# Optimization experiments

Measured on AMD Instinct MI355X. Metric: run time of the kernel, lower is better.

Reference implementation:

```python
import jax, jax.numpy as jnp
import numpy as np

N_NODES = 100000


def gcn_conv(x, edge_index, W, b, n_nodes):
    """PyG GCNConv: add self-loops, symmetric deg^-1/2 normalization,
    linear transform, scatter-add aggregate, bias."""
    src, dst = edge_index[0], edge_index[1]
    # add self-loops
    loop = jnp.arange(n_nodes, dtype=edge_index.dtype)
    src = jnp.concatenate([src, loop])
    dst = jnp.concatenate([dst, loop])
    # transform first (in_dim >= out_dim ordering used by PyG)
    h = x @ W  # [N, out]
    # symmetric normalization from in-degree (incl. self-loops)
    ones = jnp.ones(src.shape[0], dtype=x.dtype)
    deg = jax.ops.segment_sum(ones, dst, num_segments=n_nodes)
    dinv = jnp.where(deg > 0, jax.lax.rsqrt(deg), 0.0).astype(x.dtype)
    norm = dinv[src] * dinv[dst]  # [E+N]
    msg = h[src] * norm[:, None]  # gather + scale
    out = jax.ops.segment_sum(msg, dst, num_segments=n_nodes)
    return out + b


def setup_inputs() -> dict:
    key = jax.random.key(0)
    k1, k2, k3, k4 = jax.random.split(key, 4)
    n, e = N_NODES, 1600000
    d_in, d_hid, n_cls = 256, 256, 64
    x = jax.random.normal(k1, (n, d_in), dtype=jnp.float32)
    edge_index = jax.random.randint(k2, (2, e), 0, n, dtype=jnp.int64)
    W1 = jax.random.normal(k3, (d_in, d_hid), dtype=jnp.float32) / np.sqrt(d_in)
    b1 = jnp.zeros((d_hid,), dtype=jnp.float32)
    W2 = jax.random.normal(k4, (d_hid, n_cls), dtype=jnp.float32) / np.sqrt(d_hid)
    b2 = jnp.zeros((n_cls,), dtype=jnp.float32)
    return {"x": x, "edge_index": edge_index, "W1": W1, "b1": b1, "W2": W2, "b2": b2}


def reference(x, edge_index, W1, b1, W2, b2):
    n = x.shape[0]
    h = jax.nn.relu(gcn_conv(x, edge_index, W1, b1, n))
    # dropout is identity in eval mode (training=False)
    logits = gcn_conv(h, edge_index, W2, b2, n)
    return jax.nn.log_softmax(logits, axis=1)
```

## Files before the change

kernel.cpp:

```cpp
#include <hip/hip_runtime.h>
#include <math.h>


typedef __attribute__((ext_vector_type(8))) short bf16x8;
typedef __attribute__((ext_vector_type(4))) float f32x4;

__device__ inline unsigned short f2bf(float f) {
    union { float f; unsigned int u; } v; v.f = f;
    unsigned int r = v.u + 0x7fffu + ((v.u >> 16) & 1u);
    return (unsigned short)(r >> 16);
}
__device__ inline float bf2f_lo(unsigned int u) {
    union { unsigned int u; float f; } v; v.u = u << 16; return v.f;
}
__device__ inline float bf2f_hi(unsigned int u) {
    union { unsigned int u; float f; } v; v.u = u & 0xffff0000u; return v.f;
}

__device__ inline void acc8(float* acc, uint4 q, float w) {
    acc[0] += bf2f_lo(q.x) * w; acc[1] += bf2f_hi(q.x) * w;
    acc[2] += bf2f_lo(q.y) * w; acc[3] += bf2f_hi(q.y) * w;
    acc[4] += bf2f_lo(q.z) * w; acc[5] += bf2f_hi(q.z) * w;
    acc[6] += bf2f_lo(q.w) * w; acc[7] += bf2f_hi(q.w) * w;
}

__global__ __launch_bounds__(256) void deg_rank_kernel(
    const int* __restrict__ dst, int E, int* __restrict__ cnt,
    int* __restrict__ rank) {
    int e = blockIdx.x * blockDim.x + threadIdx.x;
    if (e < E) rank[e] = atomicAdd(&cnt[dst[e]], 1);
}

__global__ __launch_bounds__(256) void scan_part1_kernel(
    const int* __restrict__ cnt, int* __restrict__ bsum, int N) {
    __shared__ int s[256];
    const int tid = threadIdx.x;
    int base = blockIdx.x * 1024 + tid * 4;
    int v = 0;
#pragma unroll
    for (int j = 0; j < 4; ++j)
        if (base + j < N) v += cnt[base + j];
    s[tid] = v;
    __syncthreads();
    for (int off = 128; off > 0; off >>= 1) {
        if (tid < off) s[tid] += s[tid + off];
        __syncthreads();
    }
    if (tid == 0) bsum[blockIdx.x] = s[0];
}

__global__ __launch_bounds__(1024) void scan_part2_kernel(
    const int* __restrict__ bsum, int* __restrict__ boffs, int NB,
    int* __restrict__ row_ptr, int N) {
    __shared__ int s[1024];
    const int tid = threadIdx.x;
    int v = (tid < NB) ? bsum[tid] : 0;
    s[tid] = v;
    __syncthreads();
    for (int off = 1; off < 1024; off <<= 1) {
        int t = (tid >= off) ? s[tid - off] : 0;
        __syncthreads();
        if (tid >= off) s[tid] += t;
        __syncthreads();
    }
    if (tid < NB) boffs[tid] = s[tid] - v;
    if (tid == 1023) row_ptr[N] = s[1023];
}

__global__ __launch_bounds__(256) void scan_part3_kernel(
    const int* __restrict__ cnt, const int* __restrict__ boffs,
    int* __restrict__ row_ptr, int N) {
    __shared__ int s[256];
    const int tid = threadIdx.x;
    int base = blockIdx.x * 1024 + tid * 4;
    int c[4];
    int v = 0;
#pragma unroll
    for (int j = 0; j < 4; ++j) {
        c[j] = (base + j < N) ? cnt[base + j] : 0;
        v += c[j];
    }
    s[tid] = v;
    __syncthreads();
    for (int off = 1; off < 256; off <<= 1) {
        int t = (tid >= off) ? s[tid - off] : 0;
        __syncthreads();
        if (tid >= off) s[tid] += t;
        __syncthreads();
    }
    int run = boffs[blockIdx.x] + s[tid] - v;
#pragma unroll
    for (int j = 0; j < 4; ++j) {
        if (base + j < N) {
            row_ptr[base + j] = run;
            run += c[j];
        }
    }
}

__global__ __launch_bounds__(256) void scatter_kernel(
    const int* __restrict__ src, const int* __restrict__ dst,
    const int* __restrict__ rank, const int* __restrict__ cnt,
    const int* __restrict__ row_ptr, int2* __restrict__ csr_ew, int E) {
    int e = blockIdx.x * blockDim.x + threadIdx.x;
    if (e >= E) return;
    int s = src[e], d = dst[e];
    float w = rsqrtf((float)cnt[s] + 1.0f) * rsqrtf((float)cnt[d] + 1.0f);
    int pos = row_ptr[d] + rank[e];
    int2 rec;
    rec.x = s;
    rec.y = __float_as_int(w);
    csr_ew[pos] = rec;
}

__global__ __launch_bounds__(256) void castw_kernel(
    const float* __restrict__ W1, const float* __restrict__ W2,
    unsigned short* __restrict__ W1t, unsigned short* __restrict__ W2t) {
    int i = blockIdx.x * 256 + threadIdx.x;
    if (i < 65536) {
        int n = i >> 8, k = i & 255;
        W1t[i] = f2bf(W1[(size_t)k * 256 + n]);
    } else if (i < 65536 + 16384) {
        int j = i - 65536;
        int n = j >> 8, k = j & 255;
        W2t[j] = f2bf(W2[(size_t)k * 64 + n]);
    }
}

__global__ __launch_bounds__(256) void gemm1_kernel(
    const float* __restrict__ A, const unsigned short* __restrict__ Bt,
    unsigned short* __restrict__ C, int M) {
    __shared__ unsigned short As[128][32];
    __shared__ unsigned short Bs[256][32];

    const int tid = threadIdx.x;
    const int wave = tid >> 6, lane = tid & 63;
    const int quad = lane >> 4, l15 = lane & 15;
    const int m0 = blockIdx.x * 128;

    f32x4 acc[8][4] = {};

    const int arow = tid >> 1;
    const int akk  = (tid & 1) << 4;
    const int gr = m0 + arow;

    for (int k0 = 0; k0 < 256; k0 += 32) {
        float4 a0 = make_float4(0.f,0.f,0.f,0.f), a1 = a0, a2 = a0, a3 = a0;
        if (gr < M) {
            const float* ap = &A[(size_t)gr * 256 + k0 + akk];
            a0 = *(const float4*)&ap[0];
            a1 = *(const float4*)&ap[4];
            a2 = *(const float4*)&ap[8];
            a3 = *(const float4*)&ap[12];
        }
        bf16x8 av0, av1;
        av0[0] = (short)f2bf(a0.x); av0[1] = (short)f2bf(a0.y);
        av0[2] = (short)f2bf(a0.z); av0[3] = (short)f2bf(a0.w);
        av0[4] = (short)f2bf(a1.x); av0[5] = (short)f2bf(a1.y);
        av0[6] = (short)f2bf(a1.z); av0[7] = (short)f2bf(a1.w);
        av1[0] = (short)f2bf(a2.x); av1[1] = (short)f2bf(a2.y);
        av1[2] = (short)f2bf(a2.z); av1[3] = (short)f2bf(a2.w);
        av1[4] = (short)f2bf(a3.x); av1[5] = (short)f2bf(a3.y);
        av1[6] = (short)f2bf(a3.z); av1[7] = (short)f2bf(a3.w);
        *(bf16x8*)&As[arow][akk]     = av0;
        *(bf16x8*)&As[arow][akk + 8] = av1;

        const unsigned short* bsrc = &Bt[(size_t)tid * 256 + k0];
        *(bf16x8*)&Bs[tid][0]  = *(const bf16x8*)&bsrc[0];
        *(bf16x8*)&Bs[tid][8]  = *(const bf16x8*)&bsrc[8];
        *(bf16x8*)&Bs[tid][16] = *(const bf16x8*)&bsrc[16];
        *(bf16x8*)&Bs[tid][24] = *(const bf16x8*)&bsrc[24];
        __syncthreads();

        bf16x8 bfv[4];
#pragma unroll
        for (int nt = 0; nt < 4; ++nt)
            bfv[nt] = *(const bf16x8*)&Bs[wave * 64 + nt * 16 + l15][quad * 8];
#pragma unroll
        for (int mt = 0; mt < 8; ++mt) {
            bf16x8 af = *(const bf16x8*)&As[mt * 16 + l15][quad * 8];
#pragma unroll
            for (int nt = 0; nt < 4; ++nt)
                acc[mt][nt] = __builtin_amdgcn_mfma_f32_16x16x32_bf16(
                    af, bfv[nt], acc[mt][nt], 0, 0, 0);
        }
        __syncthreads();
    }

#pragma unroll
    for (int mt = 0; mt < 8; ++mt) {
#pragma unroll
        for (int nt = 0; nt < 4; ++nt) {
            int gcol = wave * 64 + nt * 16 + l15;
#pragma unroll
            for (int r = 0; r < 4; ++r) {
                int grow = m0 + mt * 16 + quad * 4 + r;
                if (grow < M)
                    C[(size_t)grow * 256 + gcol] = f2bf(acc[mt][nt][r]);
            }
        }
    }
}

__global__ __launch_bounds__(256) void aggfused_kernel(
    const uint4* __restrict__ h,
    const int2* __restrict__ ew,
    const int* __restrict__ row_ptr, const int* __restrict__ cnt,
    const float* __restrict__ bias, const unsigned short* __restrict__ W2t,
    unsigned short* __restrict__ h2b, int N) {
    __shared__ unsigned short As[16][264];

    const int tid = threadIdx.x;
    const int wave = tid >> 6, lane = tid & 63;
    const int half = lane >> 5;
    const int c = lane & 31;
    const int node0 = blockIdx.x * 16;

    for (int i = 0; i < 4; ++i) {
        const int local = wave * 4 + i;
        const int node = node0 + local;
        float acc[8] = {0.f, 0.f, 0.f, 0.f, 0.f, 0.f, 0.f, 0.f};
        if (node < N) {
            float dv = rsqrtf((float)cnt[node] + 1.0f);
            float w0 = dv * dv;
            uint4 qs = h[(size_t)node * 32 + c];
            const int beg = row_ptr[node], end = row_ptr[node + 1];
            acc8(acc, qs, half == 0 ? w0 : 0.f);
            if (beg < end) {
                const int last = end - 1;
                int2 r0 = ew[min(beg + half,     last)];
                int2 r1 = ew[min(beg + 2 + half, last)];
                int2 r2 = ew[min(beg + 4 + half, last)];
                int2 r3 = ew[min(beg + 6 + half, last)];
                for (int e = beg; e < end; e += 8) {
                    float we0 = (e + half     < end) ? __int_as_float(r0.y) : 0.f;
                    float we1 = (e + 2 + half < end) ? __int_as_float(r1.y) : 0.f;
                    float we2 = (e + 4 + half < end) ? __int_as_float(r2.y) : 0.f;
                    float we3 = (e + 6 + half < end) ? __int_as_float(r3.y) : 0.f;
                    uint4 q0 = h[(size_t)r0.x * 32 + c];
                    uint4 q1 = h[(size_t)r1.x * 32 + c];
                    uint4 q2 = h[(size_t)r2.x * 32 + c];
                    uint4 q3 = h[(size_t)r3.x * 32 + c];
                    const int en = e + 8;
                    int2 n0 = ew[min(en + half,     last)];
                    int2 n1 = ew[min(en + 2 + half, last)];
                    int2 n2 = ew[min(en + 4 + half, last)];
                    int2 n3 = ew[min(en + 6 + half, last)];
                    acc8(acc, q0, we0);
                    acc8(acc, q1, we1);
                    acc8(acc, q2, we2);
                    acc8(acc, q3, we3);
                    r0 = n0; r1 = n1; r2 = n2; r3 = n3;
                }
            }
        }
#pragma unroll
        for (int k = 0; k < 8; ++k) acc[k] += __shfl_xor(acc[k], 32, 64);

        if (half == 0) {
            float4 b0 = *(const float4*)&bias[c * 8];
            float4 b1 = *(const float4*)&bias[c * 8 + 4];
            unsigned int o0 = f2bf(fmaxf(acc[0] + b0.x, 0.f));
            unsigned int o1 = f2bf(fmaxf(acc[1] + b0.y, 0.f));
            unsigned int o2 = f2bf(fmaxf(acc[2] + b0.z, 0.f));
            unsigned int o3 = f2bf(fmaxf(acc[3] + b0.w, 0.f));
            unsigned int o4 = f2bf(fmaxf(acc[4] + b1.x, 0.f));
            unsigned int o5 = f2bf(fmaxf(acc[5] + b1.y, 0.f));
            unsigned int o6 = f2bf(fmaxf(acc[6] + b1.z, 0.f));
            unsigned int o7 = f2bf(fmaxf(acc[7] + b1.w, 0.f));
            uint4 ov;
            ov.x = o0 | (o1 << 16);
            ov.y = o2 | (o3 << 16);
            ov.z = o4 | (o5 << 16);
            ov.w = o6 | (o7 << 16);
            *(uint4*)&As[local][c * 8] = ov;
        }
    }
    __syncthreads();

    const int quad = lane >> 4, l15 = lane & 15;
    f32x4 accd = {};
#pragma unroll
    for (int k0 = 0; k0 < 8; ++k0) {
        bf16x8 af = *(const bf16x8*)&As[l15][k0 * 32 + quad * 8];
        bf16x8 bf = *(const bf16x8*)&W2t[(size_t)(wave * 16 + l15) * 256 +
                                         k0 * 32 + quad * 8];
        accd = __builtin_amdgcn_mfma_f32_16x16x32_bf16(af, bf, accd, 0, 0, 0);
    }
#pragma unroll
    for (int r = 0; r < 4; ++r) {
        int node = node0 + quad * 4 + r;
        if (node < N)
            h2b[(size_t)node * 64 + wave * 16 + l15] = f2bf(accd[r]);
    }
}

__global__ __launch_bounds__(256) void agg64_kernel(
    const uint4* __restrict__ h,
    const int2* __restrict__ ew, const int* __restrict__ row_ptr,
    const int* __restrict__ cnt, const float* __restrict__ bias,
    float* __restrict__ out, int N) {
    const int node = blockIdx.x * 4 + (threadIdx.x >> 6);
    if (node >= N) return;
    const int lane = threadIdx.x & 63;
    const int g = lane >> 3;
    const int c = lane & 7;

    float dv = rsqrtf((float)cnt[node] + 1.0f);
    float w0 = dv * dv;

    float acc[8] = {0.f, 0.f, 0.f, 0.f, 0.f, 0.f, 0.f, 0.f};
    {
        uint4 q = h[(size_t)node * 8 + c];
        acc8(acc, q, g == 0 ? w0 : 0.f);
    }

    const int beg = row_ptr[node], end = row_ptr[node + 1];
    if (beg < end) {
        const int last = end - 1;
        int2 r0 = ew[min(beg + g,     last)];
        int2 r1 = ew[min(beg + 8 + g, last)];
        for (int e = beg; e < end; e += 16) {
            float wa = (e + g     < end) ? __int_as_float(r0.y) : 0.f;
            float wb = (e + 8 + g < end) ? __int_as_float(r1.y) : 0.f;
            uint4 q0 = h[(size_t)r0.x * 8 + c];
            uint4 q1 = h[(size_t)r1.x * 8 + c];
            const int en = e + 16;
            int2 n0 = ew[min(en + g,     last)];
            int2 n1 = ew[min(en + 8 + g, last)];
            acc8(acc, q0, wa);
            acc8(acc, q1, wb);
            r0 = n0; r1 = n1;
        }
    }

#pragma unroll
    for (int k = 0; k < 8; ++k) {
        acc[k] += __shfl_xor(acc[k], 8, 64);
        acc[k] += __shfl_xor(acc[k], 16, 64);
        acc[k] += __shfl_xor(acc[k], 32, 64);
    }

    float4 b0 = *(const float4*)&bias[c * 8];
    float4 b1 = *(const float4*)&bias[c * 8 + 4];
    float v[8];
    v[0] = acc[0] + b0.x; v[1] = acc[1] + b0.y;
    v[2] = acc[2] + b0.z; v[3] = acc[3] + b0.w;
    v[4] = acc[4] + b1.x; v[5] = acc[5] + b1.y;
    v[6] = acc[6] + b1.z; v[7] = acc[7] + b1.w;

    float m = v[0];
#pragma unroll
    for (int k = 1; k < 8; ++k) m = fmaxf(m, v[k]);
    m = fmaxf(m, __shfl_xor(m, 1, 64));
    m = fmaxf(m, __shfl_xor(m, 2, 64));
    m = fmaxf(m, __shfl_xor(m, 4, 64));
    float s = 0.f;
#pragma unroll
    for (int k = 0; k < 8; ++k) s += expf(v[k] - m);
    s += __shfl_xor(s, 1, 64);
    s += __shfl_xor(s, 2, 64);
    s += __shfl_xor(s, 4, 64);
    float ls = m + logf(s);

    if (g == 0) {
        float4 o0, o1;
        o0.x = v[0] - ls; o0.y = v[1] - ls; o0.z = v[2] - ls; o0.w = v[3] - ls;
        o1.x = v[4] - ls; o1.y = v[5] - ls; o1.z = v[6] - ls; o1.w = v[7] - ls;
        *(float4*)&out[(size_t)node * 64 + c * 8] = o0;
        *(float4*)&out[(size_t)node * 64 + c * 8 + 4] = o1;
    }
}

extern "C" void kernel_launch(void* const* d_in, const int* in_sizes, int n_in,
                              void* d_out, int out_size, void* d_ws, size_t ws_size,
                              hipStream_t stream) {
    const float* x  = (const float*)d_in[0];
    const int*   ei = (const int*)d_in[1];
    const float* W1 = (const float*)d_in[2];
    const float* b1 = (const float*)d_in[3];
    const float* W2 = (const float*)d_in[4];
    const float* b2 = (const float*)d_in[5];
    float* out = (float*)d_out;

    const int N = in_sizes[0] / 256;
    const int E = in_sizes[1] / 2;
    const int NP = 102400;
    const int NB = (N + 1023) / 1024;

    char* ws = (char*)d_ws;
    int*   cnt     = (int*)ws;                 ws += (size_t)NP * 4;
    int*   rank    = (int*)ws;                 ws += (size_t)E * 4;
    int*   row_ptr = (int*)ws;                 ws += (size_t)(NP + 4) * 4;
    int*   bsum    = (int*)ws;                 ws += (size_t)1024 * 4;
    int*   boffs   = (int*)ws;                 ws += (size_t)1024 * 4;
    int2*  csr_ew  = (int2*)ws;                ws += (size_t)E * 8;
    unsigned short* W1t   = (unsigned short*)ws; ws += (size_t)256 * 256 * 2;
    unsigned short* W2t   = (unsigned short*)ws; ws += (size_t)256 * 64 * 2;
    unsigned short* h1b   = (unsigned short*)ws; ws += (size_t)N * 256 * 2;
    unsigned short* h2b   = (unsigned short*)ws; ws += (size_t)N * 64 * 2;

    hipMemsetAsync(cnt, 0, (size_t)N * sizeof(int), stream);

    deg_rank_kernel<<<(E + 255) / 256, 256, 0, stream>>>(ei + E, E, cnt, rank);
    scan_part1_kernel<<<NB, 256, 0, stream>>>(cnt, bsum, N);
    scan_part2_kernel<<<1, 1024, 0, stream>>>(bsum, boffs, NB, row_ptr, N);
    scan_part3_kernel<<<NB, 256, 0, stream>>>(cnt, boffs, row_ptr, N);
    scatter_kernel<<<(E + 255) / 256, 256, 0, stream>>>(
        ei, ei + E, rank, cnt, row_ptr, csr_ew, E);

    castw_kernel<<<(65536 + 16384 + 255) / 256, 256, 0, stream>>>(W1, W2, W1t, W2t);

    gemm1_kernel<<<(N + 127) / 128, 256, 0, stream>>>(x, W1t, h1b, N);

    aggfused_kernel<<<(N + 15) / 16, 256, 0, stream>>>(
        (const uint4*)h1b, csr_ew, row_ptr, cnt, b1, W2t, h2b, N);

    agg64_kernel<<<(N + 3) / 4, 256, 0, stream>>>(
        (const uint4*)h2b, csr_ew, row_ptr, cnt, b2, out, N);
}
```

Before: 539.2 us.

## Fold symmetric normalization into GEMM epilogue and drop per-edge weights

Precomputes deg^-1/2 once per node during the scan, then pre-scales the transformed features by the source-node factor in the GEMM and layer-1 epilogues. The destination factor is applied once per node after aggregation. This removes the per-edge weight from the CSR, halving edge-record bandwidth to plain int source indices. Padding is handled with a zeroed dummy row N instead of clamped indices, and nontemporal loads and stores are added on streaming accesses. The trade-off is that bf16 rounding now happens on pre-scaled values, and the zero row must be written each call.

```diff
diff --git a/kernel.cpp b/kernel.cpp
--- a/kernel.cpp
+++ b/kernel.cpp
@@ -17,18 +17,22 @@
     union { unsigned int u; float f; } v; v.u = u & 0xffff0000u; return v.f;
 }
 
-__device__ inline void acc8(float* acc, uint4 q, float w) {
-    acc[0] += bf2f_lo(q.x) * w; acc[1] += bf2f_hi(q.x) * w;
-    acc[2] += bf2f_lo(q.y) * w; acc[3] += bf2f_hi(q.y) * w;
-    acc[4] += bf2f_lo(q.z) * w; acc[5] += bf2f_hi(q.z) * w;
-    acc[6] += bf2f_lo(q.w) * w; acc[7] += bf2f_hi(q.w) * w;
+__device__ inline void acc8a(float* acc, uint4 q) {
+    acc[0] += bf2f_lo(q.x); acc[1] += bf2f_hi(q.x);
+    acc[2] += bf2f_lo(q.y); acc[3] += bf2f_hi(q.y);
+    acc[4] += bf2f_lo(q.z); acc[5] += bf2f_hi(q.z);
+    acc[6] += bf2f_lo(q.w); acc[7] += bf2f_hi(q.w);
 }
 
 __global__ __launch_bounds__(256) void deg_rank_kernel(
     const int* __restrict__ dst, int E, int* __restrict__ cnt,
     int* __restrict__ rank) {
     int e = blockIdx.x * blockDim.x + threadIdx.x;
-    if (e < E) rank[e] = atomicAdd(&cnt[dst[e]], 1);
+    if (e < E) {
+        int d = __builtin_nontemporal_load(&dst[e]);
+        int r = atomicAdd(&cnt[d], 1);
+        __builtin_nontemporal_store(r, &rank[e]);
+    }
 }
 
 __global__ __launch_bounds__(256) void scan_part1_kernel(
@@ -69,7 +73,7 @@
 
 __global__ __launch_bounds__(256) void scan_part3_kernel(
     const int* __restrict__ cnt, const int* __restrict__ boffs,
-    int* __restrict__ row_ptr, int N) {
+    int* __restrict__ row_ptr, float* __restrict__ dv, int N) {
     __shared__ int s[256];
     const int tid = threadIdx.x;
     int base = blockIdx.x * 1024 + tid * 4;
@@ -93,6 +97,7 @@
     for (int j = 0; j < 4; ++j) {
         if (base + j < N) {
             row_ptr[base + j] = run;
+            dv[base + j] = rsqrtf((float)c[j] + 1.0f);
             run += c[j];
         }
     }
@@ -100,22 +105,21 @@
 
 __global__ __launch_bounds__(256) void scatter_kernel(
     const int* __restrict__ src, const int* __restrict__ dst,
-    const int* __restrict__ rank, const int* __restrict__ cnt,
-    const int* __restrict__ row_ptr, int2* __restrict__ csr_ew, int E) {
+    const int* __restrict__ rank, const int* __restrict__ row_ptr,
+    int* __restrict__ csr_src, int E) {
     int e = blockIdx.x * blockDim.x + threadIdx.x;
     if (e >= E) return;
-    int s = src[e], d = dst[e];
-    float w = rsqrtf((float)cnt[s] + 1.0f) * rsqrtf((float)cnt[d] + 1.0f);
-    int pos = row_ptr[d] + rank[e];
-    int2 rec;
-    rec.x = s;
-    rec.y = __float_as_int(w);
-    csr_ew[pos] = rec;
+    int d = __builtin_nontemporal_load(&dst[e]);
+    int s = __builtin_nontemporal_load(&src[e]);
+    int r = __builtin_nontemporal_load(&rank[e]);
+    csr_src[row_ptr[d] + r] = s;
 }
 
 __global__ __launch_bounds__(256) void castw_kernel(
     const float* __restrict__ W1, const float* __restrict__ W2,
-    unsigned short* __restrict__ W1t, unsigned short* __restrict__ W2t) {
+    unsigned short* __restrict__ W1t, unsigned short* __restrict__ W2t,
+    unsigned short* __restrict__ h1s, unsigned short* __restrict__ h2s,
+    int N) {
     int i = blockIdx.x * 256 + threadIdx.x;
     if (i < 65536) {
         int n = i >> 8, k = i & 255;
@@ -124,12 +128,16 @@
         int j = i - 65536;
         int n = j >> 8, k = j & 255;
         W2t[j] = f2bf(W2[(size_t)k * 64 + n]);
+    } else {
+        int t = i - (65536 + 16384);
+        h1s[(size_t)N * 256 + t] = 0;
+        if (t < 64) h2s[(size_t)N * 64 + t] = 0;
     }
 }
 
 __global__ __launch_bounds__(256) void gemm1_kernel(
     const float* __restrict__ A, const unsigned short* __restrict__ Bt,
-    unsigned short* __restrict__ C, int M) {
+    const float* __restrict__ dv, unsigned short* __restrict__ C, int M) {
     __shared__ unsigned short As[128][32];
     __shared__ unsigned short Bs[256][32];
 
@@ -145,23 +153,23 @@
     const int gr = m0 + arow;
 
     for (int k0 = 0; k0 < 256; k0 += 32) {
-        float4 a0 = make_float4(0.f,0.f,0.f,0.f), a1 = a0, a2 = a0, a3 = a0;
+        f32x4 a0 = {0.f, 0.f, 0.f, 0.f}, a1 = a0, a2 = a0, a3 = a0;
         if (gr < M) {
-            const float* ap = &A[(size_t)gr * 256 + k0 + akk];
-            a0 = *(const float4*)&ap[0];
-            a1 = *(const float4*)&ap[4];
-            a2 = *(const float4*)&ap[8];
-            a3 = *(const float4*)&ap[12];
+            const f32x4* ap = (const f32x4*)&A[(size_t)gr * 256 + k0 + akk];
+            a0 = __builtin_nontemporal_load(&ap[0]);
+            a1 = __builtin_nontemporal_load(&ap[1]);
+            a2 = __builtin_nontemporal_load(&ap[2]);
+            a3 = __builtin_nontemporal_load(&ap[3]);
         }
         bf16x8 av0, av1;
-        av0[0] = (short)f2bf(a0.x); av0[1] = (short)f2bf(a0.y);
-        av0[2] = (short)f2bf(a0.z); av0[3] = (short)f2bf(a0.w);
-        av0[4] = (short)f2bf(a1.x); av0[5] = (short)f2bf(a1.y);
-        av0[6] = (short)f2bf(a1.z); av0[7] = (short)f2bf(a1.w);
-        av1[0] = (short)f2bf(a2.x); av1[1] = (short)f2bf(a2.y);
-        av1[2] = (short)f2bf(a2.z); av1[3] = (short)f2bf(a2.w);
-        av1[4] = (short)f2bf(a3.x); av1[5] = (short)f2bf(a3.y);
-        av1[6] = (short)f2bf(a3.z); av1[7] = (short)f2bf(a3.w);
+        av0[0] = (short)f2bf(a0[0]); av0[1] = (short)f2bf(a0[1]);
+        av0[2] = (short)f2bf(a0[2]); av0[3] = (short)f2bf(a0[3]);
+        av0[4] = (short)f2bf(a1[0]); av0[5] = (short)f2bf(a1[1]);
+        av0[6] = (short)f2bf(a1[2]); av0[7] = (short)f2bf(a1[3]);
+        av1[0] = (short)f2bf(a2[0]); av1[1] = (short)f2bf(a2[1]);
+        av1[2] = (short)f2bf(a2[2]); av1[3] = (short)f2bf(a2[3]);
+        av1[4] = (short)f2bf(a3[0]); av1[5] = (short)f2bf(a3[1]);
+        av1[6] = (short)f2bf(a3[2]); av1[7] = (short)f2bf(a3[3]);
         *(bf16x8*)&As[arow][akk]     = av0;
         *(bf16x8*)&As[arow][akk + 8] = av1;
 
@@ -190,13 +198,14 @@
 #pragma unroll
     for (int mt = 0; mt < 8; ++mt) {
 #pragma unroll
-        for (int nt = 0; nt < 4; ++nt) {
-            int gcol = wave * 64 + nt * 16 + l15;
-#pragma unroll
-            for (int r = 0; r < 4; ++r) {
-                int grow = m0 + mt * 16 + quad * 4 + r;
-                if (grow < M)
-                    C[(size_t)grow * 256 + gcol] = f2bf(acc[mt][nt][r]);
+        for (int r = 0; r < 4; ++r) {
+            int grow = m0 + mt * 16 + quad * 4 + r;
+            if (grow < M) {
+                float sc = dv[grow];
+#pragma unroll
+                for (int nt = 0; nt < 4; ++nt)
+                    C[(size_t)grow * 256 + wave * 64 + nt * 16 + l15] =
+                        f2bf(acc[mt][nt][r] * sc);
             }
         }
     }
@@ -204,10 +213,10 @@
 
 __global__ __launch_bounds__(256) void aggfused_kernel(
     const uint4* __restrict__ h,
-    const int2* __restrict__ ew,
-    const int* __restrict__ row_ptr, const int* __restrict__ cnt,
+    const int* __restrict__ srcs,
+    const int* __restrict__ row_ptr, const float* __restrict__ dv,
     const float* __restrict__ bias, const unsigned short* __restrict__ W2t,
-    unsigned short* __restrict__ h2b, int N) {
+    unsigned short* __restrict__ h2s, int N) {
     __shared__ unsigned short As[16][264];
 
     const int tid = threadIdx.x;
@@ -220,36 +229,33 @@
         const int local = wave * 4 + i;
         const int node = node0 + local;
         float acc[8] = {0.f, 0.f, 0.f, 0.f, 0.f, 0.f, 0.f, 0.f};
+        float dvd = 0.f;
         if (node < N) {
-            float dv = rsqrtf((float)cnt[node] + 1.0f);
-            float w0 = dv * dv;
-            uint4 qs = h[(size_t)node * 32 + c];
+            dvd = dv[node];
+            uint4 qs = h[(size_t)(half == 0 ? node : N) * 32 + c];
             const int beg = row_ptr[node], end = row_ptr[node + 1];
-            acc8(acc, qs, half == 0 ? w0 : 0.f);
+            acc8a(acc, qs);
             if (beg < end) {
-                const int last = end - 1;
-                int2 r0 = ew[min(beg + half,     last)];
-                int2 r1 = ew[min(beg + 2 + half, last)];
-                int2 r2 = ew[min(beg + 4 + half, last)];
-                int2 r3 = ew[min(beg + 6 + half, last)];
+                int p0 = beg + half, p1 = beg + 2 + half,
+                    p2 = beg + 4 + half, p3 = beg + 6 + half;
+                int r0 = (p0 < end) ? __builtin_nontemporal_load(&srcs[p0]) : N;
+                int r1 = (p1 < end) ? __builtin_nontemporal_load(&srcs[p1]) : N;
+                int r2 = (p2 < end) ? __builtin_nontemporal_load(&srcs[p2]) : N;
+                int r3 = (p3 < end) ? __builtin_nontemporal_load(&srcs[p3]) : N;
                 for (int e = beg; e < end; e += 8) {
-                    float we0 = (e + half     < end) ? __int_as_float(r0.y) : 0.f;
-                    float we1 = (e + 2 + half < end) ? __int_as_float(r1.y) : 0.f;
-                    float we2 = (e + 4 + half < end) ? __int_as_float(r2.y) : 0.f;
-                    float we3 = (e + 6 + half < end) ? __int_as_float(r3.y) : 0.f;
-                    uint4 q0 = h[(size_t)r0.x * 32 + c];
-                    uint4 q1 = h[(size_t)r1.x * 32 + c];
-                    uint4 q2 = h[(size_t)r2.x * 32 + c];
-                    uint4 q3 = h[(size_t)r3.x * 32 + c];
-                    const int en = e + 8;
-                    int2 n0 = ew[min(en + half,     last)];
-                    int2 n1 = ew[min(en + 2 + half, last)];
-                    int2 n2 = ew[min(en + 4 + half, last)];
-                    int2 n3 = ew[min(en + 6 + half, last)];
-                    acc8(acc, q0, we0);
-                    acc8(acc, q1, we1);
-                    acc8(acc, q2, we2);
-                    acc8(acc, q3, we3);
+                    uint4 q0 = h[(size_t)r0 * 32 + c];
+                    uint4 q1 = h[(size_t)r1 * 32 + c];
+                    uint4 q2 = h[(size_t)r2 * 32 + c];
+                    uint4 q3 = h[(size_t)r3 * 32 + c];
+                    p0 += 8; p1 += 8; p2 += 8; p3 += 8;
+                    int n0 = (p0 < end) ? __builtin_nontemporal_load(&srcs[p0]) : N;
+                    int n1 = (p1 < end) ? __builtin_nontemporal_load(&srcs[p1]) : N;
+                    int n2 = (p2 < end) ? __builtin_nontemporal_load(&srcs[p2]) : N;
+                    int n3 = (p3 < end) ? __builtin_nontemporal_load(&srcs[p3]) : N;
+                    acc8a(acc, q0);
+                    acc8a(acc, q1);
+                    acc8a(acc, q2);
+                    acc8a(acc, q3);
                     r0 = n0; r1 = n1; r2 = n2; r3 = n3;
                 }
             }
@@ -260,14 +266,14 @@
         if (half == 0) {
             float4 b0 = *(const float4*)&bias[c * 8];
             float4 b1 = *(const float4*)&bias[c * 8 + 4];
-            unsigned int o0 = f2bf(fmaxf(acc[0] + b0.x, 0.f));
-            unsigned int o1 = f2bf(fmaxf(acc[1] + b0.y, 0.f));
-            unsigned int o2 = f2bf(fmaxf(acc[2] + b0.z, 0.f));
-            unsigned int o3 = f2bf(fmaxf(acc[3] + b0.w, 0.f));
-            unsigned int o4 = f2bf(fmaxf(acc[4] + b1.x, 0.f));
-            unsigned int o5 = f2bf(fmaxf(acc[5] + b1.y, 0.f));
-            unsigned int o6 = f2bf(fmaxf(acc[6] + b1.z, 0.f));
-            unsigned int o7 = f2bf(fmaxf(acc[7] + b1.w, 0.f));
+            unsigned int o0 = f2bf(fmaxf(acc[0] * dvd + b0.x, 0.f));
+            unsigned int o1 = f2bf(fmaxf(acc[1] * dvd + b0.y, 0.f));
+            unsigned int o2 = f2bf(fmaxf(acc[2] * dvd + b0.z, 0.f));
+            unsigned int o3 = f2bf(fmaxf(acc[3] * dvd + b0.w, 0.f));
+            unsigned int o4 = f2bf(fmaxf(acc[4] * dvd + b1.x, 0.f));
+            unsigned int o5 = f2bf(fmaxf(acc[5] * dvd + b1.y, 0.f));
+            unsigned int o6 = f2bf(fmaxf(acc[6] * dvd + b1.z, 0.f));
+            unsigned int o7 = f2bf(fmaxf(acc[7] * dvd + b1.w, 0.f));
             uint4 ov;
             ov.x = o0 | (o1 << 16);
             ov.y = o2 | (o3 << 16);
@@ -291,14 +297,15 @@
     for (int r = 0; r < 4; ++r) {
         int node = node0 + quad * 4 + r;
         if (node < N)
-            h2b[(size_t)node * 64 + wave * 16 + l15] = f2bf(accd[r]);
+            h2s[(size_t)node * 64 + wave * 16 + l15] =
+                f2bf(accd[r] * dv[node]);
     }
 }
 
 __global__ __launch_bounds__(256) void agg64_kernel(
     const uint4* __restrict__ h,
-    const int2* __restrict__ ew, const int* __restrict__ row_ptr,
-    const int* __restrict__ cnt, const float* __restrict__ bias,
+    const int* __restrict__ srcs, const int* __restrict__ row_ptr,
+    const float* __restrict__ dv, const float* __restrict__ bias,
     float* __restrict__ out, int N) {
     const int node = blockIdx.x * 4 + (threadIdx.x >> 6);
     if (node >= N) return;
@@ -306,30 +313,25 @@
     const int g = lane >> 3;
     const int c = lane & 7;
 
-    float dv = rsqrtf((float)cnt[node] + 1.0f);
-    float w0 = dv * dv;
-
     float acc[8] = {0.f, 0.f, 0.f, 0.f, 0.f, 0.f, 0.f, 0.f};
     {
-        uint4 q = h[(size_t)node * 8 + c];
-        acc8(acc, q, g == 0 ? w0 : 0.f);
+        uint4 q = h[(size_t)(g == 0 ? node : N) * 8 + c];
+        acc8a(acc, q);
     }
 
     const int beg = row_ptr[node], end = row_ptr[node + 1];
     if (beg < end) {
-        const int last = end - 1;
-        int2 r0 = ew[min(beg + g,     last)];
-        int2 r1 = ew[min(beg + 8 + g, last)];
+        int p0 = beg + g, p1 = beg + 8 + g;
+        int r0 = (p0 < end) ? __builtin_nontemporal_load(&srcs[p0]) : N;
+        int r1 = (p1 < end) ? __builtin_nontemporal_load(&srcs[p1]) : N;
         for (int e = beg; e < end; e += 16) {
-            float wa = (e + g     < end) ? __int_as_float(r0.y) : 0.f;
-            float wb = (e + 8 + g < end) ? __int_as_float(r1.y) : 0.f;
-            uint4 q0 = h[(size_t)r0.x * 8 + c];
-            uint4 q1 = h[(size_t)r1.x * 8 + c];
-            const int en = e + 16;
-            int2 n0 = ew[min(en + g,     last)];
-            int2 n1 = ew[min(en + 8 + g, last)];
-            acc8(acc, q0, wa);
-            acc8(acc, q1, wb);
+            uint4 q0 = h[(size_t)r0 * 8 + c];
+            uint4 q1 = h[(size_t)r1 * 8 + c];
+            p0 += 16; p1 += 16;
+            int n0 = (p0 < end) ? __builtin_nontemporal_load(&srcs[p0]) : N;
+            int n1 = (p1 < end) ? __builtin_nontemporal_load(&srcs[p1]) : N;
+            acc8a(acc, q0);
+            acc8a(acc, q1);
             r0 = n0; r1 = n1;
         }
     }
@@ -341,13 +343,14 @@
         acc[k] += __shfl_xor(acc[k], 32, 64);
     }
 
+    float dvd = dv[node];
     float4 b0 = *(const float4*)&bias[c * 8];
     float4 b1 = *(const float4*)&bias[c * 8 + 4];
     float v[8];
-    v[0] = acc[0] + b0.x; v[1] = acc[1] + b0.y;
-    v[2] = acc[2] + b0.z; v[3] = acc[3] + b0.w;
-    v[4] = acc[4] + b1.x; v[5] = acc[5] + b1.y;
-    v[6] = acc[6] + b1.z; v[7] = acc[7] + b1.w;
+    v[0] = acc[0] * dvd + b0.x; v[1] = acc[1] * dvd + b0.y;
+    v[2] = acc[2] * dvd + b0.z; v[3] = acc[3] * dvd + b0.w;
+    v[4] = acc[4] * dvd + b1.x; v[5] = acc[5] * dvd + b1.y;
+    v[6] = acc[6] * dvd + b1.z; v[7] = acc[7] * dvd + b1.w;
 
     float m = v[0];
 #pragma unroll
@@ -364,11 +367,10 @@
     float ls = m + logf(s);
 
     if (g == 0) {
-        float4 o0, o1;
-        o0.x = v[0] - ls; o0.y = v[1] - ls; o0.z = v[2] - ls; o0.w = v[3] - ls;
-        o1.x = v[4] - ls; o1.y = v[5] - ls; o1.z = v[6] - ls; o1.w = v[7] - ls;
-        *(float4*)&out[(size_t)node * 64 + c * 8] = o0;
-        *(float4*)&out[(size_t)node * 64 + c * 8 + 4] = o1;
+        f32x4 o0 = {v[0] - ls, v[1] - ls, v[2] - ls, v[3] - ls};
+        f32x4 o1 = {v[4] - ls, v[5] - ls, v[6] - ls, v[7] - ls};
+        __builtin_nontemporal_store(o0, (f32x4*)&out[(size_t)node * 64 + c * 8]);
+        __builtin_nontemporal_store(o1, (f32x4*)&out[(size_t)node * 64 + c * 8 + 4]);
     }
 }
 
@@ -394,28 +396,29 @@
     int*   row_ptr = (int*)ws;                 ws += (size_t)(NP + 4) * 4;
     int*   bsum    = (int*)ws;                 ws += (size_t)1024 * 4;
     int*   boffs   = (int*)ws;                 ws += (size_t)1024 * 4;
-    int2*  csr_ew  = (int2*)ws;                ws += (size_t)E * 8;
-    unsigned short* W1t   = (unsigned short*)ws; ws += (size_t)256 * 256 * 2;
-    unsigned short* W2t   = (unsigned short*)ws; ws += (size_t)256 * 64 * 2;
-    unsigned short* h1b   = (unsigned short*)ws; ws += (size_t)N * 256 * 2;
-    unsigned short* h2b   = (unsigned short*)ws; ws += (size_t)N * 64 * 2;
+    int*   csr_src = (int*)ws;                 ws += (size_t)(E + 16) * 4;
+    unsigned short* W1t = (unsigned short*)ws; ws += (size_t)256 * 256 * 2;
+    unsigned short* W2t = (unsigned short*)ws; ws += (size_t)256 * 64 * 2;
+    float* dv = (float*)ws;                    ws += (size_t)NP * 4;
+    unsigned short* h1s = (unsigned short*)ws; ws += (size_t)(N + 1) * 256 * 2;
+    unsigned short* h2s = (unsigned short*)ws; ws += (size_t)(N + 1) * 64 * 2;
 
     hipMemsetAsync(cnt, 0, (size_t)N * sizeof(int), stream);
 
     deg_rank_kernel<<<(E + 255) / 256, 256, 0, stream>>>(ei + E, E, cnt, rank);
     scan_part1_kernel<<<NB, 256, 0, stream>>>(cnt, bsum, N);
     scan_part2_kernel<<<1, 1024, 0, stream>>>(bsum, boffs, NB, row_ptr, N);
-    scan_part3_kernel<<<NB, 256, 0, stream>>>(cnt, boffs, row_ptr, N);
+    scan_part3_kernel<<<NB, 256, 0, stream>>>(cnt, boffs, row_ptr, dv, N);
     scatter_kernel<<<(E + 255) / 256, 256, 0, stream>>>(
-        ei, ei + E, rank, cnt, row_ptr, csr_ew, E);
-
-    castw_kernel<<<(65536 + 16384 + 255) / 256, 256, 0, stream>>>(W1, W2, W1t, W2t);
-
-    gemm1_kernel<<<(N + 127) / 128, 256, 0, stream>>>(x, W1t, h1b, N);
+        ei, ei + E, rank, row_ptr, csr_src, E);
+
+    castw_kernel<<<321, 256, 0, stream>>>(W1, W2, W1t, W2t, h1s, h2s, N);
+
+    gemm1_kernel<<<(N + 127) / 128, 256, 0, stream>>>(x, W1t, dv, h1s, N);
 
     aggfused_kernel<<<(N + 15) / 16, 256, 0, stream>>>(
-        (const uint4*)h1b, csr_ew, row_ptr, cnt, b1, W2t, h2b, N);
+        (const uint4*)h1s, csr_src, row_ptr, dv, b1, W2t, h2s, N);
 
     agg64_kernel<<<(N + 3) / 4, 256, 0, stream>>>(
-        (const uint4*)h2b, csr_ew, row_ptr, cnt, b2, out, N);
-}
+        (const uint4*)h2s, csr_src, row_ptr, dv, b2, out, N);
+}
```

Result: slower. 578.5 us (+7.3%).
